# Optimization experiments

Measured on AMD Instinct MI355X. Metric: run time of the kernel, lower is better.

Reference implementation:

```python
import math
import jax, jax.numpy as jnp
import numpy as np

N_HEADS = 16


def setup_inputs() -> dict:
    key = jax.random.key(0)
    k1, k2 = jax.random.split(key)
    # qkv: [N, H*C, T] queries; y: [N, H*C, S] keys/values (k = v = y)
    qkv = jax.random.normal(k1, (2, 1024, 2048), dtype=jnp.float32)
    y = jax.random.normal(k2, (2, 1024, 2048), dtype=jnp.float32)
    return {"qkv": qkv, "y": y}


def reference(qkv, y):
    bs, width, length = qkv.shape
    ch = width // N_HEADS  # head dim = 64
    q = qkv.reshape(bs * N_HEADS, ch, length)          # [B*H, C, T]
    k = v = y.reshape(bs * N_HEADS, ch, -1)            # [B*H, C, S]
    scale = 1.0 / math.sqrt(math.sqrt(ch))             # applied to both q and k
    weight = jnp.einsum('bct,bcs->bts', q * scale, k * scale)  # [B*H, T, S]
    weight = jax.nn.softmax(weight.astype(jnp.float32), axis=-1).astype(weight.dtype)
    a = jnp.einsum('bts,bcs->bct', weight, v)          # [B*H, C, T]
    return a.reshape(bs, -1, length)                   # [N, H*C, T]
```

## Files before the change

kernel.cpp:

```cpp
#include <hip/hip_runtime.h>
#include <hip/hip_bf16.h>


typedef __attribute__((ext_vector_type(4))) float f32x4;
typedef __attribute__((ext_vector_type(8))) short bf16x8;
typedef __attribute__((ext_vector_type(4))) float float4_t;

__device__ __forceinline__ unsigned short f2bf(float f) {
  unsigned u = __builtin_bit_cast(unsigned, f);
  u += 0x7FFFu + ((u >> 16) & 1u);
  return (unsigned short)(u >> 16);
}

#if __has_builtin(__builtin_amdgcn_exp2f)
#define EXP2F(x) __builtin_amdgcn_exp2f(x)
#else
#define EXP2F(x) __expf((x) * 0.6931471805599453f)
#endif

__device__ __forceinline__ unsigned pack_bf2(float a, float b) {
  unsigned short lo = __builtin_bit_cast(unsigned short, __float2bfloat16(a));
  unsigned short hi = __builtin_bit_cast(unsigned short, __float2bfloat16(b));
  return (unsigned)lo | ((unsigned)hi << 16);
}

#define GLOAD_LDS16(g, l) __builtin_amdgcn_global_load_lds(                 \
    (const __attribute__((address_space(1))) unsigned*)(g),                 \
    (__attribute__((address_space(3))) unsigned*)(l), 16, 0, 0)

#define SCL (0.35355339059327373f * 1.2011224087864498f)

__global__ __launch_bounds__(256)
void prep(const float* __restrict__ qkv, const float* __restrict__ y,
          unsigned short* __restrict__ kT, unsigned short* __restrict__ v,
          unsigned short* __restrict__ qT) {
  __shared__ unsigned short tb[64][66];
  const int tid = threadIdx.x;
  const int isQ = blockIdx.x >> 10;
  const int b2  = blockIdx.x & 1023;
  const int bh  = b2 >> 5;
  const int s0  = (b2 & 31) * 64;
  const float* src = (isQ ? qkv : y) + (size_t)bh * 131072;

  const int c = tid >> 2, j = tid & 3;
  float fv[16];
  #pragma unroll
  for (int p = 0; p < 4; ++p) {
    float4_t a = *(const float4_t*)(src + c * 2048 + s0 + j * 16 + p * 4);
    #pragma unroll
    for (int i = 0; i < 4; ++i) fv[p * 4 + i] = a[i];
  }
  if (!isQ) {
    bf16x8 u0, u1;
    #pragma unroll
    for (int i = 0; i < 8; ++i) { u0[i] = (short)f2bf(fv[i]); u1[i] = (short)f2bf(fv[8 + i]); }
    unsigned short* vp = v + (size_t)bh * 131072 + c * 2048 + s0 + j * 16;
    *(bf16x8*)(vp) = u0;
    *(bf16x8*)(vp + 8) = u1;
  }
  #pragma unroll
  for (int m = 0; m < 8; ++m) {
    unsigned lo = f2bf(fv[2 * m] * SCL);
    unsigned hi = f2bf(fv[2 * m + 1] * SCL);
    *(unsigned*)&tb[c][j * 16 + 2 * m] = lo | (hi << 16);
  }
  __syncthreads();

  const int srow = tid >> 2, i2 = tid & 3;
  unsigned short outv[16];
  #pragma unroll
  for (int m = 0; m < 16; ++m) outv[m] = tb[i2 * 16 + m][srow];
  unsigned short* dT = (isQ ? qT : kT) + (size_t)bh * 131072 +
                       (size_t)(s0 + srow) * 64 + i2 * 16;
  *(bf16x8*)(dT)     = *(bf16x8*)&outv[0];
  *(bf16x8*)(dT + 8) = *(bf16x8*)&outv[8];
}

#define KOFF0 0
#define KOFF1 8192
#define VOFF0 16384
#define VOFF1 24576
#define POFF  32768
#define PSTR  176
#define LDS_MAIN 55296

__global__ __launch_bounds__(512, 4)
void attn_main(const unsigned short* __restrict__ kT,
               const unsigned short* __restrict__ v,
               const unsigned short* __restrict__ qT,
               float* __restrict__ out) {
  __shared__ __align__(16) char smem[LDS_MAIN];
  const int tid  = threadIdx.x;
  const int lane = tid & 63;
  const int w    = tid >> 6;
  const int c15  = lane & 15;
  const int g    = lane >> 4;
  const int bh   = blockIdx.x >> 4;
  const int t0   = (blockIdx.x & 15) * 128;

  const unsigned short* kg = kT + (size_t)bh * 131072;
  const unsigned short* vg = v  + (size_t)bh * 131072;
  float*                og = out + (size_t)bh * 131072;

  bf16x8 qf0, qf1;
  {
    const unsigned short* qp = qT + (size_t)bh * 131072 +
                               (size_t)(t0 + w * 16 + c15) * 64 + 8 * g;
    qf0 = *(const bf16x8*)(qp);
    qf1 = *(const bf16x8*)(qp + 32);
  }

  const int sr = tid >> 3, sb = tid & 7;
  const int ss = sb ^ (sr & 7);
  const unsigned short* kbase = kg + sr * 64 + ss * 8;
  const unsigned short* vbase = vg + sr * 2048 + ss * 8;
  char* const slds = smem + tid * 16;

  f32x4 oacc[4];
  #pragma unroll
  for (int nc = 0; nc < 4; ++nc) oacc[nc] = (f32x4){0.f, 0.f, 0.f, 0.f};
  float lsum = 0.f;

  char* const prow = smem + POFF + w * (16 * PSTR) + c15 * PSTR;
  char* const pbw  = prow + 8 * g;
  char* const pbr  = prow + 16 * g;

  GLOAD_LDS16(kbase, slds + KOFF0);
  GLOAD_LDS16(vbase, slds + VOFF0);
  __syncthreads();

  auto tile = [&](int koff, int voff, int nkoff, int nvoff, int it) {
    if (it + 1 < 32) {
      GLOAD_LDS16(kbase + (it + 1) * 4096, slds + nkoff);
      GLOAD_LDS16(vbase + (it + 1) * 64,   slds + nvoff);
    }
    char* kb = smem + koff;
    char* vb = smem + voff;

    f32x4 accs[4];
    #pragma unroll
    for (int nt = 0; nt < 4; ++nt) accs[nt] = (f32x4){0.f, 0.f, 0.f, 0.f};
    #pragma unroll
    for (int kt = 0; kt < 2; ++kt)
      #pragma unroll
      for (int nt = 0; nt < 4; ++nt) {
        const int srow = nt * 16 + c15;
        bf16x8 kf = *(bf16x8*)(kb + srow * 128 + (((kt * 4 + g) ^ (srow & 7)) * 16));
        accs[nt] = __builtin_amdgcn_mfma_f32_16x16x32_bf16(kf, kt ? qf1 : qf0,
                                                           accs[nt], 0, 0, 0);
      }

    #pragma unroll
    for (int nt = 0; nt < 4; ++nt) {
      float p0 = EXP2F(accs[nt][0]);
      float p1 = EXP2F(accs[nt][1]);
      float p2 = EXP2F(accs[nt][2]);
      float p3 = EXP2F(accs[nt][3]);
      lsum += (p0 + p1) + (p2 + p3);
      *(unsigned*)(pbw + 32 * nt)     = pack_bf2(p0, p1);
      *(unsigned*)(pbw + 32 * nt + 4) = pack_bf2(p2, p3);
    }
    __builtin_amdgcn_sched_barrier(0);

    #pragma unroll
    for (int kt = 0; kt < 2; ++kt) {
      bf16x8 pf = *(bf16x8*)(pbr + 64 * kt);
      #pragma unroll
      for (int nc = 0; nc < 4; ++nc) {
        const int crow = nc * 16 + c15;
        bf16x8 vf = *(bf16x8*)(vb + crow * 128 + (((kt * 4 + g) ^ (crow & 7)) * 16));
        oacc[nc] = __builtin_amdgcn_mfma_f32_16x16x32_bf16(pf, vf, oacc[nc], 0, 0, 0);
      }
    }
    __syncthreads();
  };

  #pragma unroll 1
  for (int it2 = 0; it2 < 16; ++it2) {
    tile(KOFF0, VOFF0, KOFF1, VOFF1, 2 * it2);
    tile(KOFF1, VOFF1, KOFF0, VOFF0, 2 * it2 + 1);
  }

  lsum += __shfl_xor(lsum, 16);
  lsum += __shfl_xor(lsum, 32);
  const float invl = 1.0f / lsum;

  float* ep = (float*)smem;
  float* lp = (float*)(smem + 33792);
  if (lane < 16) lp[w * 16 + c15] = invl;
  #pragma unroll
  for (int nc = 0; nc < 4; ++nc)
    #pragma unroll
    for (int r = 0; r < 4; ++r)
      ep[(nc * 16 + c15) * 132 + (w * 16 + 4 * g + r)] = oacc[nc][r];
  __syncthreads();
  const int t4 = tid & 31;
  const int c0 = tid >> 5;
  float4_t il4 = *(float4_t*)(lp + t4 * 4);
  #pragma unroll
  for (int itr = 0; itr < 4; ++itr) {
    int cc = itr * 16 + c0;
    float4_t o = *(float4_t*)(ep + cc * 132 + t4 * 4);
    o *= il4;
    *(float4_t*)(og + cc * 2048 + t0 + t4 * 4) = o;
  }
}

#define LDS_K 0
#define LDS_V 8192
#define LDS_P 16384
#define LDS_TOTAL 27648

__global__ __launch_bounds__(256)
void attn_fwd(const float* __restrict__ qkv, const float* __restrict__ y,
              float* __restrict__ out) {
  __shared__ __align__(16) char smem[LDS_TOTAL];
  const int tid  = threadIdx.x;
  const int lane = tid & 63;
  const int w    = tid >> 6;
  const int c15  = lane & 15;
  const int g    = lane >> 4;
  const int bh = blockIdx.x >> 5;
  const int t0 = (blockIdx.x & 31) * 64;
  const float* qg = qkv + (size_t)bh * 64 * 2048;
  const float* kg = y   + (size_t)bh * 64 * 2048;
  float*       og = out + (size_t)bh * 64 * 2048;
  const float SC = 0.35355339059327373f;
  bf16x8 qf[2];
  {
    const int tq = t0 + w * 16 + c15;
    #pragma unroll
    for (int kt = 0; kt < 2; ++kt)
      #pragma unroll
      for (int j = 0; j < 8; ++j)
        qf[kt][j] = (short)f2bf(qg[(kt * 32 + 8 * g + j) * 2048 + tq] * SC);
  }
  f32x4 oacc[4];
  #pragma unroll
  for (int nc = 0; nc < 4; ++nc) oacc[nc] = (f32x4){0.f, 0.f, 0.f, 0.f};
  float m_run[4], l_run[4];
  #pragma unroll
  for (int r = 0; r < 4; ++r) { m_run[r] = -1e30f; l_run[r] = 0.f; }
  const int ks_row = tid & 63, ks_cb = tid >> 6;
  const int vs_c = tid >> 2, vs_j = tid & 3;
  for (int it = 0; it < 32; ++it) {
    const int s0 = it * 64;
    #pragma unroll
    for (int pass = 0; pass < 2; ++pass) {
      const int cblk = pass * 4 + ks_cb;
      bf16x8 pk;
      #pragma unroll
      for (int i = 0; i < 8; ++i)
        pk[i] = (short)f2bf(kg[(cblk * 8 + i) * 2048 + s0 + ks_row] * SC);
      *(bf16x8*)(smem + LDS_K + ks_row * 128 + ((cblk ^ (ks_row & 7)) * 16)) = pk;
    }
    #pragma unroll
    for (int pass = 0; pass < 2; ++pass) {
      const int sblk = pass * 4 + vs_j;
      const float4_t a = *(const float4_t*)(kg + vs_c * 2048 + s0 + sblk * 8);
      const float4_t b = *(const float4_t*)(kg + vs_c * 2048 + s0 + sblk * 8 + 4);
      bf16x8 pv;
      #pragma unroll
      for (int i = 0; i < 4; ++i) { pv[i] = (short)f2bf(a[i]); pv[4 + i] = (short)f2bf(b[i]); }
      *(bf16x8*)(smem + LDS_V + vs_c * 128 + ((sblk ^ (vs_c & 7)) * 16)) = pv;
    }
    __syncthreads();
    f32x4 accs[4];
    #pragma unroll
    for (int nt = 0; nt < 4; ++nt) accs[nt] = (f32x4){0.f, 0.f, 0.f, 0.f};
    #pragma unroll
    for (int kt = 0; kt < 2; ++kt)
      #pragma unroll
      for (int nt = 0; nt < 4; ++nt) {
        const int srow = nt * 16 + c15;
        bf16x8 kf = *(bf16x8*)(smem + LDS_K + srow * 128 +
                               (((kt * 4 + g) ^ (srow & 7)) * 16));
        accs[nt] = __builtin_amdgcn_mfma_f32_16x16x32_bf16(qf[kt], kf, accs[nt], 0, 0, 0);
      }
    float mt[4];
    #pragma unroll
    for (int r = 0; r < 4; ++r)
      mt[r] = fmaxf(fmaxf(accs[0][r], accs[1][r]), fmaxf(accs[2][r], accs[3][r]));
    #pragma unroll
    for (int off = 1; off <= 8; off <<= 1)
      #pragma unroll
      for (int r = 0; r < 4; ++r) mt[r] = fmaxf(mt[r], __shfl_xor(mt[r], off));
    float alpha[4];
    #pragma unroll
    for (int r = 0; r < 4; ++r) {
      float mn = fmaxf(m_run[r], mt[r]);
      alpha[r] = __expf(m_run[r] - mn);
      m_run[r] = mn;
    }
    float ls[4] = {0.f, 0.f, 0.f, 0.f};
    #pragma unroll
    for (int nt = 0; nt < 4; ++nt)
      #pragma unroll
      for (int r = 0; r < 4; ++r) {
        float p = __expf(accs[nt][r] - m_run[r]);
        accs[nt][r] = p;
        ls[r] += p;
      }
    #pragma unroll
    for (int off = 1; off <= 8; off <<= 1)
      #pragma unroll
      for (int r = 0; r < 4; ++r) ls[r] += __shfl_xor(ls[r], off);
    #pragma unroll
    for (int r = 0; r < 4; ++r) l_run[r] = l_run[r] * alpha[r] + ls[r];
    #pragma unroll
    for (int nc = 0; nc < 4; ++nc)
      #pragma unroll
      for (int r = 0; r < 4; ++r) oacc[nc][r] *= alpha[r];
    char* pb = smem + LDS_P + w * 2816;
    #pragma unroll
    for (int nt = 0; nt < 4; ++nt)
      #pragma unroll
      for (int r = 0; r < 4; ++r)
        *(unsigned short*)(pb + (4 * g + r) * 176 + (nt * 16 + c15) * 2) =
            f2bf(accs[nt][r]);
    __builtin_amdgcn_sched_barrier(0);
    #pragma unroll
    for (int kt = 0; kt < 2; ++kt) {
      bf16x8 pf = *(bf16x8*)(pb + c15 * 176 + (kt * 32 + 8 * g) * 2);
      #pragma unroll
      for (int nc = 0; nc < 4; ++nc) {
        const int crow = nc * 16 + c15;
        bf16x8 vf = *(bf16x8*)(smem + LDS_V + crow * 128 +
                               (((kt * 4 + g) ^ (crow & 7)) * 16));
        oacc[nc] = __builtin_amdgcn_mfma_f32_16x16x32_bf16(pf, vf, oacc[nc], 0, 0, 0);
      }
    }
    __syncthreads();
  }
  float inv_l[4];
  #pragma unroll
  for (int r = 0; r < 4; ++r) inv_l[r] = 1.0f / l_run[r];
  float* ep = (float*)smem;
  #pragma unroll
  for (int nc = 0; nc < 4; ++nc)
    #pragma unroll
    for (int r = 0; r < 4; ++r)
      ep[(nc * 16 + c15) * 68 + (w * 16 + 4 * g + r)] = oacc[nc][r] * inv_l[r];
  __syncthreads();
  #pragma unroll
  for (int itr = 0; itr < 4; ++itr) {
    int idx = itr * 256 + tid;
    int cc  = idx >> 4;
    int v4  = idx & 15;
    float4_t o = *(float4_t*)(ep + cc * 68 + v4 * 4);
    *(float4_t*)(og + cc * 2048 + t0 + v4 * 4) = o;
  }
}

extern "C" void kernel_launch(void* const* d_in, const int* in_sizes, int n_in,
                              void* d_out, int out_size, void* d_ws, size_t ws_size,
                              hipStream_t stream) {
  const float* qkv = (const float*)d_in[0];
  const float* y   = (const float*)d_in[1];
  float*       out = (float*)d_out;
  if (ws_size < (size_t)25165824) {
    attn_fwd<<<dim3(1024), dim3(256), 0, stream>>>(qkv, y, out);
    return;
  }
  unsigned short* kT = (unsigned short*)d_ws;
  unsigned short* vv = kT + 4194304;
  unsigned short* qT = kT + 8388608;
  prep<<<dim3(2048), dim3(256), 0, stream>>>(qkv, y, kT, vv, qT);
  attn_main<<<dim3(512), dim3(512), 0, stream>>>(kT, vv, qT, out);
}
```

Measured before the change: 62.84 us.

## Double query rows per wave and keep P in registers via permlane swaps

Each wave now handles 32 query rows (two 16-row groups) against the same K/V LDS tiles, so every K/V fragment read feeds two MFMAs. The P matrix no longer goes through LDS. The operands are swapped so the score accumulator layout can be turned into the B operand with v_permlane32/16_swap, which removes the LDS stores and reads. Block-to-head mapping is remapped, the grid is halved to 256 blocks, the epilogue writes output directly without an LDS transpose, and launch bounds drop to 2 blocks. The cost is higher register pressure and fewer blocks (256 on a 256-CU part), which cuts latency hiding. The direct output stores are also less coalesced.

```diff
diff --git a/kernel.cpp b/kernel.cpp
--- a/kernel.cpp
+++ b/kernel.cpp
@@ -5,6 +5,7 @@
 typedef __attribute__((ext_vector_type(4))) float f32x4;
 typedef __attribute__((ext_vector_type(8))) short bf16x8;
 typedef __attribute__((ext_vector_type(4))) float float4_t;
+typedef __attribute__((ext_vector_type(4))) unsigned u32x4;
 
 __device__ __forceinline__ unsigned short f2bf(float f) {
   unsigned u = __builtin_bit_cast(unsigned, f);
@@ -80,11 +81,9 @@
 #define KOFF1 8192
 #define VOFF0 16384
 #define VOFF1 24576
-#define POFF  32768
-#define PSTR  176
-#define LDS_MAIN 55296
-
-__global__ __launch_bounds__(512, 4)
+#define LDS_MAIN 32768
+
+__global__ __launch_bounds__(512, 2)
 void attn_main(const unsigned short* __restrict__ kT,
                const unsigned short* __restrict__ v,
                const unsigned short* __restrict__ qT,
@@ -95,19 +94,23 @@
   const int w    = tid >> 6;
   const int c15  = lane & 15;
   const int g    = lane >> 4;
-  const int bh   = blockIdx.x >> 4;
-  const int t0   = (blockIdx.x & 15) * 128;
+
+  const int bid = blockIdx.x;
+  const int bh  = (bid & 7) * 4 + ((bid >> 3) & 3);
+  const int t0  = (bid >> 5) * 256;
 
   const unsigned short* kg = kT + (size_t)bh * 131072;
   const unsigned short* vg = v  + (size_t)bh * 131072;
   float*                og = out + (size_t)bh * 131072;
 
-  bf16x8 qf0, qf1;
+  bf16x8 qf[2][2];
   {
-    const unsigned short* qp = qT + (size_t)bh * 131072 +
-                               (size_t)(t0 + w * 16 + c15) * 64 + 8 * g;
-    qf0 = *(const bf16x8*)(qp);
-    qf1 = *(const bf16x8*)(qp + 32);
+    const unsigned short* qp0 = qT + (size_t)bh * 131072 +
+                                (size_t)(t0 + w * 32 + c15) * 64 + 8 * g;
+    qf[0][0] = *(const bf16x8*)(qp0);
+    qf[0][1] = *(const bf16x8*)(qp0 + 32);
+    qf[1][0] = *(const bf16x8*)(qp0 + 1024);
+    qf[1][1] = *(const bf16x8*)(qp0 + 1024 + 32);
   }
 
   const int sr = tid >> 3, sb = tid & 7;
@@ -116,14 +119,12 @@
   const unsigned short* vbase = vg + sr * 2048 + ss * 8;
   char* const slds = smem + tid * 16;
 
-  f32x4 oacc[4];
-  #pragma unroll
-  for (int nc = 0; nc < 4; ++nc) oacc[nc] = (f32x4){0.f, 0.f, 0.f, 0.f};
-  float lsum = 0.f;
-
-  char* const prow = smem + POFF + w * (16 * PSTR) + c15 * PSTR;
-  char* const pbw  = prow + 8 * g;
-  char* const pbr  = prow + 16 * g;
+  f32x4 oacc[2][4];
+  #pragma unroll
+  for (int tg = 0; tg < 2; ++tg)
+    #pragma unroll
+    for (int nc = 0; nc < 4; ++nc) oacc[tg][nc] = (f32x4){0.f, 0.f, 0.f, 0.f};
+  float lsum[2] = {0.f, 0.f};
 
   GLOAD_LDS16(kbase, slds + KOFF0);
   GLOAD_LDS16(vbase, slds + VOFF0);
@@ -137,41 +138,57 @@
     char* kb = smem + koff;
     char* vb = smem + voff;
 
-    f32x4 accs[4];
-    #pragma unroll
-    for (int nt = 0; nt < 4; ++nt) accs[nt] = (f32x4){0.f, 0.f, 0.f, 0.f};
+    f32x4 acc[2][4];
+    #pragma unroll
+    for (int tg = 0; tg < 2; ++tg)
+      #pragma unroll
+      for (int nt = 0; nt < 4; ++nt) acc[tg][nt] = (f32x4){0.f, 0.f, 0.f, 0.f};
     #pragma unroll
     for (int kt = 0; kt < 2; ++kt)
       #pragma unroll
       for (int nt = 0; nt < 4; ++nt) {
         const int srow = nt * 16 + c15;
         bf16x8 kf = *(bf16x8*)(kb + srow * 128 + (((kt * 4 + g) ^ (srow & 7)) * 16));
-        accs[nt] = __builtin_amdgcn_mfma_f32_16x16x32_bf16(kf, kt ? qf1 : qf0,
-                                                           accs[nt], 0, 0, 0);
-      }
-
-    #pragma unroll
-    for (int nt = 0; nt < 4; ++nt) {
-      float p0 = EXP2F(accs[nt][0]);
-      float p1 = EXP2F(accs[nt][1]);
-      float p2 = EXP2F(accs[nt][2]);
-      float p3 = EXP2F(accs[nt][3]);
-      lsum += (p0 + p1) + (p2 + p3);
-      *(unsigned*)(pbw + 32 * nt)     = pack_bf2(p0, p1);
-      *(unsigned*)(pbw + 32 * nt + 4) = pack_bf2(p2, p3);
-    }
-    __builtin_amdgcn_sched_barrier(0);
-
-    #pragma unroll
-    for (int kt = 0; kt < 2; ++kt) {
-      bf16x8 pf = *(bf16x8*)(pbr + 64 * kt);
+        acc[0][nt] = __builtin_amdgcn_mfma_f32_16x16x32_bf16(kf, qf[0][kt], acc[0][nt], 0, 0, 0);
+        acc[1][nt] = __builtin_amdgcn_mfma_f32_16x16x32_bf16(kf, qf[1][kt], acc[1][nt], 0, 0, 0);
+      }
+
+    bf16x8 pa[2][2];
+    #pragma unroll
+    for (int tg = 0; tg < 2; ++tg) {
+      unsigned W[8];
+      #pragma unroll
+      for (int nt = 0; nt < 4; ++nt) {
+        float p0 = EXP2F(acc[tg][nt][0]);
+        float p1 = EXP2F(acc[tg][nt][1]);
+        float p2 = EXP2F(acc[tg][nt][2]);
+        float p3 = EXP2F(acc[tg][nt][3]);
+        lsum[tg] += (p0 + p1) + (p2 + p3);
+        W[nt * 2]     = pack_bf2(p0, p1);
+        W[nt * 2 + 1] = pack_bf2(p2, p3);
+      }
+      #pragma unroll
+      for (int kt = 0; kt < 2; ++kt) {
+        unsigned a0 = W[kt * 4 + 0], b0 = W[kt * 4 + 2];
+        unsigned a1 = W[kt * 4 + 1], b1 = W[kt * 4 + 3];
+        asm volatile("v_permlane32_swap_b32 %0, %1" : "+v"(a0), "+v"(b0));
+        asm volatile("v_permlane32_swap_b32 %0, %1" : "+v"(a1), "+v"(b1));
+        asm volatile("v_permlane16_swap_b32 %0, %1" : "+v"(a0), "+v"(b0));
+        asm volatile("v_permlane16_swap_b32 %0, %1" : "+v"(a1), "+v"(b1));
+        u32x4 fw = {a0, a1, b0, b1};
+        pa[tg][kt] = __builtin_bit_cast(bf16x8, fw);
+      }
+    }
+
+    #pragma unroll
+    for (int kt = 0; kt < 2; ++kt)
       #pragma unroll
       for (int nc = 0; nc < 4; ++nc) {
         const int crow = nc * 16 + c15;
         bf16x8 vf = *(bf16x8*)(vb + crow * 128 + (((kt * 4 + g) ^ (crow & 7)) * 16));
-        oacc[nc] = __builtin_amdgcn_mfma_f32_16x16x32_bf16(pf, vf, oacc[nc], 0, 0, 0);
-      }
-    }
+        oacc[0][nc] = __builtin_amdgcn_mfma_f32_16x16x32_bf16(vf, pa[0][kt], oacc[0][nc], 0, 0, 0);
+        oacc[1][nc] = __builtin_amdgcn_mfma_f32_16x16x32_bf16(vf, pa[1][kt], oacc[1][nc], 0, 0, 0);
+      }
     __syncthreads();
   };
 
@@ -181,29 +198,22 @@
     tile(KOFF1, VOFF1, KOFF0, VOFF0, 2 * it2 + 1);
   }
 
-  lsum += __shfl_xor(lsum, 16);
-  lsum += __shfl_xor(lsum, 32);
-  const float invl = 1.0f / lsum;
-
-  float* ep = (float*)smem;
-  float* lp = (float*)(smem + 33792);
-  if (lane < 16) lp[w * 16 + c15] = invl;
+  #pragma unroll
+  for (int tg = 0; tg < 2; ++tg) {
+    lsum[tg] += __shfl_xor(lsum[tg], 16);
+    lsum[tg] += __shfl_xor(lsum[tg], 32);
+  }
+  const float invl0 = 1.0f / lsum[0];
+  const float invl1 = 1.0f / lsum[1];
+
+  float* ob = og + t0 + w * 32 + c15 + (size_t)(4 * g) * 2048;
   #pragma unroll
   for (int nc = 0; nc < 4; ++nc)
     #pragma unroll
-    for (int r = 0; r < 4; ++r)
-      ep[(nc * 16 + c15) * 132 + (w * 16 + 4 * g + r)] = oacc[nc][r];
-  __syncthreads();
-  const int t4 = tid & 31;
-  const int c0 = tid >> 5;
-  float4_t il4 = *(float4_t*)(lp + t4 * 4);
-  #pragma unroll
-  for (int itr = 0; itr < 4; ++itr) {
-    int cc = itr * 16 + c0;
-    float4_t o = *(float4_t*)(ep + cc * 132 + t4 * 4);
-    o *= il4;
-    *(float4_t*)(og + cc * 2048 + t0 + t4 * 4) = o;
-  }
+    for (int r = 0; r < 4; ++r) {
+      ob[(size_t)(nc * 16 + r) * 2048]      = oacc[0][nc][r] * invl0;
+      ob[(size_t)(nc * 16 + r) * 2048 + 16] = oacc[1][nc][r] * invl1;
+    }
 }
 
 #define LDS_K 0
@@ -366,5 +376,5 @@
   unsigned short* vv = kT + 4194304;
   unsigned short* qT = kT + 8388608;
   prep<<<dim3(2048), dim3(256), 0, stream>>>(qkv, y, kT, vv, qT);
-  attn_main<<<dim3(512), dim3(512), 0, stream>>>(kT, vv, qT, out);
-}
+  attn_main<<<dim3(256), dim3(512), 0, stream>>>(kT, vv, qT, out);
+}
```

After: 60.27 us. 4.1% less time.
